# Kernel tuning notes

Measured on AMD Instinct MI355X. Metric: run time of the kernel, lower is better.

The kernel has to match this reference:

```python
import jax, jax.numpy as jnp
import numpy as np

B, K, PS, DP = 8, 8, 128, 16           # batch, patches/example, patch px, dino patch size
D, NH, HD, L = 1024, 8, 128, 2         # embed dim, heads, head dim, transformer layers
GRID = PS // DP                        # 8 tokens per side
TPP = GRID * GRID                      # 64 tokens per patch


def _conv(x, w, stride, pad):
    return jax.lax.conv_general_dilated(x, w, (stride, stride), pad,
                                        dimension_numbers=('NCHW', 'OIHW', 'NCHW'))


def _ln(x, g, b, eps=1e-5):
    m = jnp.mean(x, -1, keepdims=True)
    v = jnp.var(x, -1, keepdims=True)
    return (x - m) * jax.lax.rsqrt(v + eps) * g + b


def _bn(x, g, b, m, v, eps=1e-5):
    inv = jax.lax.rsqrt(v + eps)
    return (x - m[:, None, None]) * inv[:, None, None] * g[:, None, None] + b[:, None, None]


def _up2(x):  # bilinear x2, align_corners=False (half-pixel, matches jax.image.resize)
    n, c, h, w = x.shape
    return jax.image.resize(x, (n, c, 2 * h, 2 * w), method='linear')


def _mha(x, wqkv, bqkv, wo, bo):
    b, s, d = x.shape
    qkv = x @ wqkv.T + bqkv
    q, k, v = jnp.split(qkv, 3, axis=-1)
    q = q.reshape(b, s, NH, HD).transpose(0, 2, 1, 3)
    k = k.reshape(b, s, NH, HD).transpose(0, 2, 1, 3)
    v = v.reshape(b, s, NH, HD).transpose(0, 2, 1, 3)
    att = jax.nn.softmax(jnp.einsum('bhqd,bhkd->bhqk', q, k) / jnp.sqrt(jnp.float32(HD)), axis=-1)
    o = jnp.einsum('bhqk,bhkd->bhqd', att, v).transpose(0, 2, 1, 3).reshape(b, s, d)
    return o @ wo.T + bo


def setup_inputs() -> dict:
    key = jax.random.key(0)
    ks = iter(jax.random.split(key, 40))

    def rn(shape, s=0.02):
        return jax.random.normal(next(ks), shape, jnp.float32) * s

    inp = {}
    inp['patches'] = jax.random.normal(next(ks), (B, K, 3, PS, PS), jnp.float32)
    inp['pe_w'] = rn((D, 3, DP, DP))
    inp['pe_b'] = jnp.zeros((D,), jnp.float32)
    inp['qkv_w'] = rn((L, 3 * D, D))
    inp['qkv_b'] = jnp.zeros((L, 3 * D), jnp.float32)
    inp['out_w'] = rn((L, D, D))
    inp['out_b'] = jnp.zeros((L, D), jnp.float32)
    inp['ln1_g'] = jnp.ones((L, D), jnp.float32)
    inp['ln1_b'] = jnp.zeros((L, D), jnp.float32)
    inp['ff1_w'] = rn((L, 4 * D, D))
    inp['ff1_b'] = jnp.zeros((L, 4 * D), jnp.float32)
    inp['ff2_w'] = rn((L, D, 4 * D))
    inp['ff2_b'] = jnp.zeros((L, D), jnp.float32)
    inp['ln2_g'] = jnp.ones((L, D), jnp.float32)
    inp['ln2_b'] = jnp.zeros((L, D), jnp.float32)
    chans = [(512, D), (256, 512), (128, 256), (64, 128)]
    for i, (co, ci) in enumerate(chans, 1):
        inp[f'dw{i}'] = rn((co, ci, 3, 3), 0.05)
        inp[f'db{i}'] = jnp.zeros((co,), jnp.float32)
        inp[f'g{i}'] = jnp.ones((co,), jnp.float32)
        inp[f'be{i}'] = jnp.zeros((co,), jnp.float32)
        inp[f'm{i}'] = jnp.zeros((co,), jnp.float32)
        inp[f'v{i}'] = jnp.ones((co,), jnp.float32)
    inp['dw5'] = rn((1, 64, 1, 1), 0.05)
    inp['db5'] = jnp.zeros((1,), jnp.float32)
    return inp


def reference(patches, pe_w, pe_b, qkv_w, qkv_b, out_w, out_b, ln1_g, ln1_b,
              ff1_w, ff1_b, ff2_w, ff2_b, ln2_g, ln2_b,
              dw1, db1, g1, be1, m1, v1, dw2, db2, g2, be2, m2, v2,
              dw3, db3, g3, be3, m3, v3, dw4, db4, g4, be4, m4, v4, dw5, db5):
    b, k = patches.shape[:2]
    x = patches.reshape(b * k, 3, PS, PS)
    # frozen DINO patch embedding (runs under torch.no_grad in the original)
    hs = _conv(x, pe_w, DP, 'VALID') + pe_b[None, :, None, None]     # [BK, D, GRID, GRID]
    hs = jax.lax.stop_gradient(hs)
    hs = hs.reshape(b * k, D, TPP).transpose(0, 2, 1).reshape(b, k * TPP, D)
    # post-norm TransformerEncoder (norm_first=False, gelu), dropout=eval (identity)
    for i in range(L):
        hs = _ln(hs + _mha(hs, qkv_w[i], qkv_b[i], out_w[i], out_b[i]), ln1_g[i], ln1_b[i])
        ff = jax.nn.gelu(hs @ ff1_w[i].T + ff1_b[i], approximate=False) @ ff2_w[i].T + ff2_b[i]
        hs = _ln(hs + ff, ln2_g[i], ln2_b[i])
    fm = hs.reshape(b * k, TPP, D).transpose(0, 2, 1).reshape(b * k, D, GRID, GRID)
    # CNN decoder: (conv3x3 -> BN(eval) -> ReLU -> bilinear x2) x4 -> conv1x1
    y = _up2(jax.nn.relu(_bn(_conv(fm, dw1, 1, 'SAME') + db1[None, :, None, None], g1, be1, m1, v1)))
    y = _up2(jax.nn.relu(_bn(_conv(y, dw2, 1, 'SAME') + db2[None, :, None, None], g2, be2, m2, v2)))
    y = _up2(jax.nn.relu(_bn(_conv(y, dw3, 1, 'SAME') + db3[None, :, None, None], g3, be3, m3, v3)))
    y = _up2(jax.nn.relu(_bn(_conv(y, dw4, 1, 'SAME') + db4[None, :, None, None], g4, be4, m4, v4)))
    y = _conv(y, dw5, 1, 'VALID') + db5[None, :, None, None]          # [BK, 1, PS, PS]
    return y.reshape(b, k, 1, PS, PS)
```

## Files before the change

kernel.cpp:

```cpp
#include <hip/hip_runtime.h>
#include <stdint.h>


typedef unsigned short u16;
typedef __bf16 bf16x8 __attribute__((ext_vector_type(8)));
typedef short  s16x8  __attribute__((ext_vector_type(8)));
typedef float  f32x4  __attribute__((ext_vector_type(4)));

__device__ __forceinline__ float b2f(u16 x) { return __uint_as_float(((unsigned)x) << 16); }
__device__ __forceinline__ u16 f2b(float f) {
  unsigned u = __float_as_uint(f);
  unsigned r = (u + 0x7fffu + ((u >> 16) & 1u)) >> 16;
  return (u16)r;
}
__device__ __forceinline__ void async16(u16* lds, const u16* g) {
  __builtin_amdgcn_global_load_lds((const __attribute__((address_space(1))) void*)g,
                                   (__attribute__((address_space(3))) void*)lds, 16, 0, 0);
}
__device__ __forceinline__ float gelu_f(float x) {
  return 0.5f * x * (1.0f + erff(x * 0.70710678118654752f));
}

__global__ __launch_bounds__(256) void cvt_f2b(const float* __restrict__ src,
                                               u16* __restrict__ dst, int n) {
  const int i = (blockIdx.x * 256 + threadIdx.x) * 4;
  if (i + 3 < n) {
    const float4 v = *(const float4*)(src + i);
    dst[i] = f2b(v.x); dst[i + 1] = f2b(v.y); dst[i + 2] = f2b(v.z); dst[i + 3] = f2b(v.w);
  }
}

__global__ __launch_bounds__(256) void gemm_bt(
    const u16* __restrict__ A, int lda, long long sAb, long long sAh,
    const u16* __restrict__ B, int ldb, long long sBb, long long sBh,
    u16* __restrict__ Cb, int ldc, long long sCb, long long sCh,
    const float* __restrict__ bias, int epi, int ZH, int nk)
{
  __shared__ u16 As[128 * 32];
  __shared__ u16 Bs[128 * 32];
  const int tid = threadIdx.x;
  const int zb = blockIdx.z / ZH, zh = blockIdx.z % ZH;
  const u16* Ab = A + zb * sAb + zh * sAh;
  const u16* Bb = B + zb * sBb + zh * sBh;
  const int m0 = blockIdx.y << 7, n0 = blockIdx.x << 7;
  const int wave = tid >> 6, lane = tid & 63;
  const int wm = (wave >> 1) << 6, wn = (wave & 1) << 6;
  const int lr = lane & 15, lq = lane >> 4;
  const int rowb = tid >> 2, kc = (tid & 3) << 3;

  f32x4 acc[4][4] = {};

  for (int kt = 0; kt < nk; ++kt) {
    const int k0 = kt << 5;
    __syncthreads();
    async16(&As[tid * 8],         Ab + (long long)(m0 + rowb)      * lda + (k0 + kc));
    async16(&As[(tid + 256) * 8], Ab + (long long)(m0 + rowb + 64) * lda + (k0 + kc));
    async16(&Bs[tid * 8],         Bb + (long long)(n0 + rowb)      * ldb + (k0 + kc));
    async16(&Bs[(tid + 256) * 8], Bb + (long long)(n0 + rowb + 64) * ldb + (k0 + kc));
    __syncthreads();

    bf16x8 af[4], bfv[4];
#pragma unroll
    for (int mi = 0; mi < 4; ++mi)
      af[mi] = __builtin_bit_cast(bf16x8, *(const s16x8*)&As[((wm + mi * 16 + lr) << 5) + (lq << 3)]);
#pragma unroll
    for (int ni = 0; ni < 4; ++ni)
      bfv[ni] = __builtin_bit_cast(bf16x8, *(const s16x8*)&Bs[((wn + ni * 16 + lr) << 5) + (lq << 3)]);
#pragma unroll
    for (int mi = 0; mi < 4; ++mi)
#pragma unroll
      for (int ni = 0; ni < 4; ++ni)
        acc[mi][ni] = __builtin_amdgcn_mfma_f32_16x16x32_bf16(af[mi], bfv[ni], acc[mi][ni], 0, 0, 0);
  }

  const long long Co = zb * sCb + zh * sCh;
#pragma unroll
  for (int ni = 0; ni < 4; ++ni) {
    const int col = n0 + wn + ni * 16 + lr;
    const float badd = bias ? bias[col] : 0.0f;
#pragma unroll
    for (int mi = 0; mi < 4; ++mi) {
      const int row0 = m0 + wm + mi * 16 + (lq << 2);
#pragma unroll
      for (int r = 0; r < 4; ++r) {
        float v = acc[mi][ni][r] + badd;
        if (epi == 1) v = gelu_f(v);
        Cb[Co + (long long)(row0 + r) * ldc + col] = f2b(v);
      }
    }
  }
}

__global__ __launch_bounds__(256) void conv_gemm(
    const u16* __restrict__ U, const u16* __restrict__ Wr,
    u16* __restrict__ Out,
    const float* __restrict__ bn_g, const float* __restrict__ bn_b,
    const float* __restrict__ bn_m, const float* __restrict__ bn_v,
    const float* __restrict__ cb,
    const u16* __restrict__ zpg,
    int H, int W, int l2w, int l2hw, int l2c, int CoutReal, int Kdim, int nk)
{
  __shared__ u16 As[128 * 32];
  __shared__ u16 Bs[128 * 32];
  const int tid = threadIdx.x;
  const int m0 = blockIdx.y << 7, n0 = blockIdx.x << 7;
  const int wave = tid >> 6, lane = tid & 63;
  const int wm = (wave >> 1) << 6, wn = (wave & 1) << 6;
  const int lr = lane & 15, lq = lane >> 4;
  const int rowb = tid >> 2, kc = (tid & 3) << 3;
  const int hwmask = (1 << l2hw) - 1, wmask = (1 << l2w) - 1, cmask = (1 << l2c) - 1;

  f32x4 acc[4][4] = {};

  for (int kt = 0; kt < nk; ++kt) {
    const int k0 = kt << 5;
    __syncthreads();
#pragma unroll
    for (int i = 0; i < 2; ++i) {
      const int mrow = m0 + rowb + (i << 6);
      const int img = mrow >> l2hw;
      const int rem = mrow & hwmask;
      const int y = rem >> l2w, x = rem & wmask;
      const int k = k0 + kc;
      const int t = k >> l2c, ci = k & cmask;
      const int dy = (t * 86) >> 8;
      const int dx = t - dy * 3;
      const int yy = y + dy - 1, xx = x + dx - 1;
      const u16* src = ((unsigned)yy < (unsigned)H && (unsigned)xx < (unsigned)W)
          ? U + ((((long long)(img << l2hw) + (yy << l2w) + xx) << l2c) + ci)
          : zpg;
      async16(&As[(tid + (i << 8)) * 8], src);
      async16(&Bs[(tid + (i << 8)) * 8], Wr + (long long)(n0 + rowb + (i << 6)) * Kdim + (k0 + kc));
    }
    __syncthreads();

    bf16x8 af[4], bfv[4];
#pragma unroll
    for (int mi = 0; mi < 4; ++mi)
      af[mi] = __builtin_bit_cast(bf16x8, *(const s16x8*)&As[((wm + mi * 16 + lr) << 5) + (lq << 3)]);
#pragma unroll
    for (int ni = 0; ni < 4; ++ni)
      bfv[ni] = __builtin_bit_cast(bf16x8, *(const s16x8*)&Bs[((wn + ni * 16 + lr) << 5) + (lq << 3)]);
#pragma unroll
    for (int mi = 0; mi < 4; ++mi)
#pragma unroll
      for (int ni = 0; ni < 4; ++ni)
        acc[mi][ni] = __builtin_amdgcn_mfma_f32_16x16x32_bf16(af[mi], bfv[ni], acc[mi][ni], 0, 0, 0);
  }

#pragma unroll
  for (int ni = 0; ni < 4; ++ni) {
    const int col = n0 + wn + ni * 16 + lr;
    const bool ok = col < CoutReal;
    float bs = 0.0f, bsh = 0.0f;
    if (ok) {
      const float inv = rsqrtf(bn_v[col] + 1e-5f);
      bs = bn_g[col] * inv;
      bsh = (cb[col] - bn_m[col]) * bs + bn_b[col];
    }
#pragma unroll
    for (int mi = 0; mi < 4; ++mi) {
      const int row0 = m0 + wm + mi * 16 + (lq << 2);
#pragma unroll
      for (int r = 0; r < 4; ++r) {
        if (ok) {
          const float v = fmaxf(acc[mi][ni][r] * bs + bsh, 0.0f);
          Out[(long long)(row0 + r) * CoutReal + col] = f2b(v);
        }
      }
    }
  }
}


__global__ void pe_gather(const float* __restrict__ patches, u16* __restrict__ Ape) {
  const int t = blockIdx.x, tid = threadIdx.x;
  const int img = t >> 6, pos = t & 63, ty = pos >> 3, tx = pos & 7;
  const float* base = patches + (long long)img * 3 * 128 * 128;
  u16* dst = Ape + (long long)t * 768;
  for (int k = tid; k < 768; k += 256) {
    const int c = k >> 8, rr = k & 255, ky = rr >> 4, kx = rr & 15;
    dst[k] = f2b(base[c * 16384 + (ty * 16 + ky) * 128 + tx * 16 + kx]);
  }
}

__global__ void vt_transpose(const u16* __restrict__ qkv, u16* __restrict__ Vt) {
  __shared__ u16 lds[64 * 130];
  const int tt = blockIdx.x;
  const int z = blockIdx.y;
  const int bq = z >> 3, h = z & 7;
  const int tid = threadIdx.x;
  for (int idx = tid; idx < 64 * 128; idx += 256) {
    const int t = idx >> 7, d = idx & 127;
    lds[t * 130 + d] = qkv[(long long)(bq * 512 + tt * 64 + t) * 3072 + 2048 + h * 128 + d];
  }
  __syncthreads();
  for (int idx = tid; idx < 64 * 128; idx += 256) {
    const int d = idx >> 6, t = idx & 63;
    Vt[(long long)z * 65536 + d * 512 + tt * 64 + t] = lds[t * 130 + d];
  }
}

__global__ __launch_bounds__(256) void softmax_rows(u16* __restrict__ P) {
  __shared__ float red[8];
  const long long base = (long long)blockIdx.x * 512;
  const int tid = threadIdx.x;
  const float sc = 0.08838834764831845f;
  float x0 = b2f(P[base + tid]) * sc;
  float x1 = b2f(P[base + tid + 256]) * sc;
  float mx = fmaxf(x0, x1);
  for (int o = 32; o; o >>= 1) mx = fmaxf(mx, __shfl_down(mx, o));
  if ((tid & 63) == 0) red[tid >> 6] = mx;
  __syncthreads();
  mx = fmaxf(fmaxf(red[0], red[1]), fmaxf(red[2], red[3]));
  const float e0 = expf(x0 - mx), e1 = expf(x1 - mx);
  float s = e0 + e1;
  for (int o = 32; o; o >>= 1) s += __shfl_down(s, o);
  __syncthreads();
  if ((tid & 63) == 0) red[tid >> 6] = s;
  __syncthreads();
  s = red[0] + red[1] + red[2] + red[3];
  const float inv = 1.0f / s;
  P[base + tid] = f2b(e0 * inv);
  P[base + tid + 256] = f2b(e1 * inv);
}

__global__ __launch_bounds__(256) void ln_kernel(
    u16* __restrict__ hsb, const u16* __restrict__ P,
    const float* __restrict__ gw, const float* __restrict__ bw)
{
  __shared__ float red[8];
  const int r = blockIdx.x, tid = threadIdx.x;
  float x[4], s = 0.0f, s2 = 0.0f;
#pragma unroll
  for (int i = 0; i < 4; ++i) {
    const int c = tid + i * 256;
    const float v = b2f(hsb[(long long)r * 1024 + c]) + b2f(P[(long long)r * 1024 + c]);
    x[i] = v; s += v; s2 += v * v;
  }
  for (int o = 32; o; o >>= 1) { s += __shfl_down(s, o); s2 += __shfl_down(s2, o); }
  if ((tid & 63) == 0) { red[tid >> 6] = s; red[4 + (tid >> 6)] = s2; }
  __syncthreads();
  s  = red[0] + red[1] + red[2] + red[3];
  s2 = red[4] + red[5] + red[6] + red[7];
  const float mean = s * (1.0f / 1024.0f);
  const float var = s2 * (1.0f / 1024.0f) - mean * mean;
  const float inv = rsqrtf(var + 1e-5f);
#pragma unroll
  for (int i = 0; i < 4; ++i) {
    const int c = tid + i * 256;
    const float y = (x[i] - mean) * inv * gw[c] + bw[c];
    hsb[(long long)r * 1024 + c] = f2b(y);
  }
}

__global__ void repack_w(const float* __restrict__ src, u16* __restrict__ dst, int Cout, int l2c) {
  const int co = blockIdx.x, tid = threadIdx.x;
  const int Cin = 1 << l2c, K9 = 9 << l2c;
  for (int j = tid; j < K9; j += 256) {
    const int t = j >> l2c, ci = j & (Cin - 1);
    u16 v = 0;
    if (co < Cout) v = f2b(src[(long long)(co * Cin + ci) * 9 + t]);
    dst[(long long)co * K9 + j] = v;
  }
}

__global__ void ups2x(const u16* __restrict__ in, u16* __restrict__ out,
                      int l2h, int l2w, int l2c, long long total)
{
  const long long idx = (long long)blockIdx.x * 256 + threadIdx.x;
  if (idx >= total) return;
  const int H = 1 << l2h, W = 1 << l2w, C = 1 << l2c;
  const int c = (int)(idx & (C - 1));
  long long t = idx >> l2c;
  const int ox = (int)(t & (2 * W - 1)); t >>= (l2w + 1);
  const int oy = (int)(t & (2 * H - 1)); t >>= (l2h + 1);
  const int img = (int)t;
  const int iy = oy >> 1, ix = ox >> 1;
  int y0, y1, x0, x1; float wy0, wy1, wx0, wx1;
  if (oy & 1) { y0 = iy; y1 = min(iy + 1, H - 1); wy0 = 0.75f; wy1 = 0.25f; }
  else        { y0 = max(iy - 1, 0); y1 = iy;     wy0 = 0.25f; wy1 = 0.75f; }
  if (ox & 1) { x0 = ix; x1 = min(ix + 1, W - 1); wx0 = 0.75f; wx1 = 0.25f; }
  else        { x0 = max(ix - 1, 0); x1 = ix;     wx0 = 0.25f; wx1 = 0.75f; }
  const u16* base = in + (((long long)img) << (l2h + l2w + l2c));
  const float v00 = b2f(base[((((long long)y0 << l2w) + x0) << l2c) + c]);
  const float v01 = b2f(base[((((long long)y0 << l2w) + x1) << l2c) + c]);
  const float v10 = b2f(base[((((long long)y1 << l2w) + x0) << l2c) + c]);
  const float v11 = b2f(base[((((long long)y1 << l2w) + x1) << l2c) + c]);
  out[idx] = f2b(wy0 * (wx0 * v00 + wx1 * v01) + wy1 * (wx0 * v10 + wx1 * v11));
}

__global__ __launch_bounds__(256) void conv1x1_final(
    const u16* __restrict__ C4, const float* __restrict__ w5,
    const float* __restrict__ b5, float* __restrict__ Z)
{
  const int tid = threadIdx.x;
  const int px = blockIdx.x * 4 + (tid >> 6);
  const int lane = tid & 63;
  float v = b2f(C4[(long long)px * 64 + lane]) * w5[lane];
  for (int o = 32; o; o >>= 1) v += __shfl_down(v, o);
  if (lane == 0) Z[px] = v + b5[0];
}

__global__ void ups_final(const float* __restrict__ Z, float* __restrict__ out) {
  const int idx = blockIdx.x * 256 + threadIdx.x;
  const int ox = idx & 127, oy = (idx >> 7) & 127, img = idx >> 14;
  const int iy = oy >> 1, ix = ox >> 1;
  int y0, y1, x0, x1; float wy0, wy1, wx0, wx1;
  if (oy & 1) { y0 = iy; y1 = min(iy + 1, 63); wy0 = 0.75f; wy1 = 0.25f; }
  else        { y0 = max(iy - 1, 0); y1 = iy;  wy0 = 0.25f; wy1 = 0.75f; }
  if (ox & 1) { x0 = ix; x1 = min(ix + 1, 63); wx0 = 0.75f; wx1 = 0.25f; }
  else        { x0 = max(ix - 1, 0); x1 = ix;  wx0 = 0.25f; wx1 = 0.75f; }
  const float* zi = Z + (long long)img * 4096;
  const float v = wy0 * (wx0 * zi[y0 * 64 + x0] + wx1 * zi[y0 * 64 + x1]) +
                  wy1 * (wx0 * zi[y1 * 64 + x0] + wx1 * zi[y1 * 64 + x1]);
  out[idx] = v;
}

extern "C" void kernel_launch(void* const* d_in, const int* in_sizes, int n_in,
                              void* d_out, int out_size, void* d_ws, size_t ws_size,
                              hipStream_t stream)
{
  (void)in_sizes; (void)n_in; (void)out_size;
  if (ws_size < 110395648u) return;
  const float* patches = (const float*)d_in[0];
  const float* pe_w = (const float*)d_in[1];
  const float* pe_b = (const float*)d_in[2];
  const float* qkv_w = (const float*)d_in[3];
  const float* qkv_b = (const float*)d_in[4];
  const float* out_w = (const float*)d_in[5];
  const float* out_b = (const float*)d_in[6];
  const float* ln1_g = (const float*)d_in[7];
  const float* ln1_b = (const float*)d_in[8];
  const float* ff1_w = (const float*)d_in[9];
  const float* ff1_b = (const float*)d_in[10];
  const float* ff2_w = (const float*)d_in[11];
  const float* ff2_b = (const float*)d_in[12];
  const float* ln2_g = (const float*)d_in[13];
  const float* ln2_b = (const float*)d_in[14];
  const float* dwv[4] = {(const float*)d_in[15], (const float*)d_in[21], (const float*)d_in[27], (const float*)d_in[33]};
  const float* dbv[4] = {(const float*)d_in[16], (const float*)d_in[22], (const float*)d_in[28], (const float*)d_in[34]};
  const float* gv[4]  = {(const float*)d_in[17], (const float*)d_in[23], (const float*)d_in[29], (const float*)d_in[35]};
  const float* bev[4] = {(const float*)d_in[18], (const float*)d_in[24], (const float*)d_in[30], (const float*)d_in[36]};
  const float* mv[4]  = {(const float*)d_in[19], (const float*)d_in[25], (const float*)d_in[31], (const float*)d_in[37]};
  const float* vv[4]  = {(const float*)d_in[20], (const float*)d_in[26], (const float*)d_in[32], (const float*)d_in[38]};
  const float* dw5 = (const float*)d_in[39];
  const float* db5 = (const float*)d_in[40];
  float* outp = (float*)d_out;
  char* ws = (char*)d_ws;

  u16* HS_B = (u16*)(ws + 0);
  u16* APE  = (u16*)(ws + 8388608);
  u16* QKV  = (u16*)(ws + 8388608);
  u16* VT   = (u16*)(ws + 33554432);
  u16* SF   = (u16*)(ws + 41943040);
  u16* FF1G = (u16*)(ws + 41943040);
  u16* ATT  = (u16*)(ws + 75497472);
  u16* P_B  = (u16*)(ws + 83886080);
  u16* W1   = (u16*)(ws + 92274688);
  u16* W2   = (u16*)(ws + 100663296);
  u16* WR1 = (u16*)(ws + 8388608);
  u16* WR2 = (u16*)(ws + 17825792);
  u16* WR3 = (u16*)(ws + 20185088);
  u16* C1  = (u16*)(ws + 20774912);
  u16* U1  = (u16*)(ws + 24969216);
  u16* C2  = (u16*)(ws + 41746432);
  u16* U2  = (u16*)(ws + 50135040);
  u16* C3  = (u16*)(ws + 83689472);
  u16* U3  = (u16*)(ws + 8388608);
  u16* C4  = (u16*)(ws + 75497472);
  u16* ZPG = (u16*)(ws + 109051904);
  u16* WR4 = (u16*)(ws + 109052160);
  float* Z = (float*)(ws + 109347072);

  pe_gather<<<4096, 256, 0, stream>>>(patches, APE);
  cvt_f2b<<<768, 256, 0, stream>>>(pe_w, W1, 786432);
  gemm_bt<<<dim3(8, 32, 1), 256, 0, stream>>>(
      APE, 768, 0, 0, W1, 768, 0, 0,
      HS_B, 1024, 0, 0, pe_b, 0, 1, 24);

  for (int l = 0; l < 2; ++l) {
    cvt_f2b<<<3072, 256, 0, stream>>>(qkv_w + (long long)l * 3145728, W1, 3145728);
    gemm_bt<<<dim3(24, 32, 1), 256, 0, stream>>>(
        HS_B, 1024, 0, 0, W1, 1024, 0, 0,
        QKV, 3072, 0, 0, qkv_b + l * 3072, 0, 1, 32);
    vt_transpose<<<dim3(8, 64), 256, 0, stream>>>(QKV, VT);
    gemm_bt<<<dim3(4, 4, 64), 256, 0, stream>>>(
        QKV, 3072, 1572864, 128, QKV + 1024, 3072, 1572864, 128,
        SF, 512, 2097152, 262144, nullptr, 0, 8, 4);
    softmax_rows<<<32768, 256, 0, stream>>>(SF);
    gemm_bt<<<dim3(1, 4, 64), 256, 0, stream>>>(
        SF, 512, 2097152, 262144, VT, 512, 524288, 65536,
        ATT, 1024, 524288, 128, nullptr, 0, 8, 16);
    cvt_f2b<<<1024, 256, 0, stream>>>(out_w + (long long)l * 1048576, W2, 1048576);
    gemm_bt<<<dim3(8, 32, 1), 256, 0, stream>>>(
        ATT, 1024, 0, 0, W2, 1024, 0, 0,
        P_B, 1024, 0, 0, out_b + l * 1024, 0, 1, 32);
    ln_kernel<<<4096, 256, 0, stream>>>(HS_B, P_B, ln1_g + l * 1024, ln1_b + l * 1024);
    cvt_f2b<<<4096, 256, 0, stream>>>(ff1_w + (long long)l * 4194304, W1, 4194304);
    cvt_f2b<<<4096, 256, 0, stream>>>(ff2_w + (long long)l * 4194304, W2, 4194304);
    gemm_bt<<<dim3(32, 32, 1), 256, 0, stream>>>(
        HS_B, 1024, 0, 0, W1, 1024, 0, 0,
        FF1G, 4096, 0, 0, ff1_b + l * 4096, 1, 1, 32);
    gemm_bt<<<dim3(8, 32, 1), 256, 0, stream>>>(
        FF1G, 4096, 0, 0, W2, 4096, 0, 0,
        P_B, 1024, 0, 0, ff2_b + l * 1024, 0, 1, 128);
    ln_kernel<<<4096, 256, 0, stream>>>(HS_B, P_B, ln2_g + l * 1024, ln2_b + l * 1024);
  }

  hipMemsetAsync((void*)ZPG, 0, 256, stream);
  repack_w<<<512, 256, 0, stream>>>(dwv[0], WR1, 512, 10);
  repack_w<<<256, 256, 0, stream>>>(dwv[1], WR2, 256, 9);
  repack_w<<<128, 256, 0, stream>>>(dwv[2], WR3, 128, 8);
  repack_w<<<128, 256, 0, stream>>>(dwv[3], WR4, 64, 7);

  conv_gemm<<<dim3(4, 32, 1), 256, 0, stream>>>(
      HS_B, WR1, C1, gv[0], bev[0], mv[0], vv[0], dbv[0], ZPG,
      8, 8, 3, 6, 10, 512, 9216, 288);
  ups2x<<<32768, 256, 0, stream>>>(C1, U1, 3, 3, 9, 8388608LL);
  conv_gemm<<<dim3(2, 128, 1), 256, 0, stream>>>(
      U1, WR2, C2, gv[1], bev[1], mv[1], vv[1], dbv[1], ZPG,
      16, 16, 4, 8, 9, 256, 4608, 144);
  ups2x<<<65536, 256, 0, stream>>>(C2, U2, 4, 4, 8, 16777216LL);
  conv_gemm<<<dim3(1, 512, 1), 256, 0, stream>>>(
      U2, WR3, C3, gv[2], bev[2], mv[2], vv[2], dbv[2], ZPG,
      32, 32, 5, 10, 8, 128, 2304, 72);
  ups2x<<<131072, 256, 0, stream>>>(C3, U3, 5, 5, 7, 33554432LL);
  conv_gemm<<<dim3(1, 2048, 1), 256, 0, stream>>>(
      U3, WR4, C4, gv[3], bev[3], mv[3], vv[3], dbv[3], ZPG,
      64, 64, 6, 12, 7, 64, 1152, 36);
  conv1x1_final<<<65536, 256, 0, stream>>>(C4, dw5, db5, Z);
  ups_final<<<4096, 256, 0, stream>>>(Z, outp);
}
```

Measured before the change: 1.503 ms.

## Triple-buffer conv_gemm LDS tiles with async loads and explicit vmcnt waits

The implicit-GEMM 3x3 convolution kernel moves from a single shared-memory tile to three buffers. Asynchronous global-to-LDS loads for K-tile t+2 are issued while tile t is being consumed. Waiting is done with explicit s_waitcnt vmcnt counts and raw s_barrier instructions instead of the two __syncthreads per iteration. This is meant to hide global load latency behind the MFMA work. In exchange it uses three times the LDS, which can lower occupancy. It also assumes nk is a multiple of 3, because the unrolled loop does not guard against tile indices past nk.

```diff
diff --git a/kernel.cpp b/kernel.cpp
--- a/kernel.cpp
+++ b/kernel.cpp
@@ -100,8 +100,8 @@
     const u16* __restrict__ zpg,
     int H, int W, int l2w, int l2hw, int l2c, int CoutReal, int Kdim, int nk)
 {
-  __shared__ u16 As[128 * 32];
-  __shared__ u16 Bs[128 * 32];
+  __shared__ u16 As[3][128 * 32];
+  __shared__ u16 Bs[3][128 * 32];
   const int tid = threadIdx.x;
   const int m0 = blockIdx.y << 7, n0 = blockIdx.x << 7;
   const int wave = tid >> 6, lane = tid & 63;
@@ -112,9 +112,8 @@
 
   f32x4 acc[4][4] = {};
 
-  for (int kt = 0; kt < nk; ++kt) {
+  auto stage = [&](int kt, int b) {
     const int k0 = kt << 5;
-    __syncthreads();
 #pragma unroll
     for (int i = 0; i < 2; ++i) {
       const int mrow = m0 + rowb + (i << 6);
@@ -129,23 +128,43 @@
       const u16* src = ((unsigned)yy < (unsigned)H && (unsigned)xx < (unsigned)W)
           ? U + ((((long long)(img << l2hw) + (yy << l2w) + xx) << l2c) + ci)
           : zpg;
-      async16(&As[(tid + (i << 8)) * 8], src);
-      async16(&Bs[(tid + (i << 8)) * 8], Wr + (long long)(n0 + rowb + (i << 6)) * Kdim + (k0 + kc));
+      async16(&As[b][(tid + (i << 8)) * 8], src);
+      async16(&Bs[b][(tid + (i << 8)) * 8], Wr + (long long)(n0 + rowb + (i << 6)) * Kdim + (k0 + kc));
     }
-    __syncthreads();
-
-    bf16x8 af[4], bfv[4];
-#pragma unroll
-    for (int mi = 0; mi < 4; ++mi)
-      af[mi] = __builtin_bit_cast(bf16x8, *(const s16x8*)&As[((wm + mi * 16 + lr) << 5) + (lq << 3)]);
-#pragma unroll
-    for (int ni = 0; ni < 4; ++ni)
-      bfv[ni] = __builtin_bit_cast(bf16x8, *(const s16x8*)&Bs[((wn + ni * 16 + lr) << 5) + (lq << 3)]);
-#pragma unroll
-    for (int mi = 0; mi < 4; ++mi)
+  };
+
+  stage(0, 0);
+  stage(1, 1);
+
+  for (int t0 = 0; t0 < nk; t0 += 3) {
+#pragma unroll
+    for (int p = 0; p < 3; ++p) {
+      const int tt = t0 + p;
+      if (tt + 2 < nk) {
+        stage(tt + 2, (p + 2) % 3);
+        asm volatile("s_waitcnt vmcnt(8)" ::: "memory");
+      } else if (tt + 1 < nk) {
+        asm volatile("s_waitcnt vmcnt(4)" ::: "memory");
+      } else {
+        asm volatile("s_waitcnt vmcnt(0)" ::: "memory");
+      }
+      asm volatile("s_barrier" ::: "memory");
+
+      bf16x8 af[4], bfv[4];
+#pragma unroll
+      for (int mi = 0; mi < 4; ++mi)
+        af[mi] = __builtin_bit_cast(bf16x8, *(const s16x8*)&As[p][((wm + mi * 16 + lr) << 5) + (lq << 3)]);
 #pragma unroll
       for (int ni = 0; ni < 4; ++ni)
-        acc[mi][ni] = __builtin_amdgcn_mfma_f32_16x16x32_bf16(af[mi], bfv[ni], acc[mi][ni], 0, 0, 0);
+        bfv[ni] = __builtin_bit_cast(bf16x8, *(const s16x8*)&Bs[p][((wn + ni * 16 + lr) << 5) + (lq << 3)]);
+#pragma unroll
+      for (int mi = 0; mi < 4; ++mi)
+#pragma unroll
+        for (int ni = 0; ni < 4; ++ni)
+          acc[mi][ni] = __builtin_amdgcn_mfma_f32_16x16x32_bf16(af[mi], bfv[ni], acc[mi][ni], 0, 0, 0);
+
+      asm volatile("s_barrier" ::: "memory");
+    }
   }
 
 #pragma unroll
```

Result: no change. 1.476 ms (-1.8%).
